# Optimization experiments

Measured on AMD Instinct MI355X. Metric: run time of the kernel, lower is better.

## Reference

```python
import jax, jax.numpy as jnp
import numpy as np

B, T = 65536, 200
H, S, P = 512, 1000, 5
EPS = 1e-6


def setup_inputs() -> dict:
    key = jax.random.key(0)
    ks = jax.random.split(key, 8)
    init = lambda k, shp, fan: (jax.random.normal(k, shp, jnp.float32) / np.float32(np.sqrt(fan)))
    return {
        "X": jax.random.randint(ks[0], (B,), 0, S, dtype=jnp.int32),
        "y": jax.random.randint(ks[1], (B, T), 0, 2, dtype=jnp.int32),
        "embed": init(ks[2], (S, H), 1.0),
        "W1": init(ks[3], (H, H), H), "b1": jnp.zeros((H,), jnp.float32),
        "W2": init(ks[4], (H, H), H), "b2": jnp.zeros((H,), jnp.float32),
        "Wout": init(ks[5], (H, P), H), "bout": jnp.zeros((P,), jnp.float32),
    }


def reference(X, y, embed, W1, b1, W2, b2, Wout, bout):
    # --- MLP over skill embeddings: params (B, 5) = (l, f, g, s, latent0) ---
    e = embed[X]                                    # (B, H)
    h = jax.nn.relu(e @ W1 + b1)                    # num_layers = 2
    h = jax.nn.relu(h @ W2 + b2)
    params = jnp.clip(jax.nn.sigmoid(h @ Wout + bout), EPS, 1.0 - EPS)  # (B, 5)
    l, g, s = params[:, 0], params[:, 2], params[:, 3]
    latent0 = params[:, 4]                          # (B,)

    y_clean = jnp.where(y == -1, 0, y).astype(jnp.float32)  # (B, T)

    # --- BKT latent-update recurrence over T steps ---
    def step(latent, y_t):
        num1 = latent * (1.0 - s)
        correct = num1 + (1.0 - latent) * g
        k_t1 = num1 / correct
        k_t0 = latent * s / (latent * s + (1.0 - latent) * (1.0 - g))
        k_t = jnp.where(y_t > 0.5, k_t1, k_t0)
        nxt = jnp.clip(k_t + (1.0 - k_t) * l, EPS, 1.0 - EPS)
        return nxt, (correct, latent)

    _, (corrects, latents) = jax.lax.scan(step, latent0, y_clean.T)  # (T, B) each
    return corrects.T, latents.T, params
```

## Files before the change

### kernel.cpp

```cpp
#include <hip/hip_runtime.h>


typedef unsigned int uint;
typedef unsigned char uchar;
typedef unsigned short ushort_t;
typedef __attribute__((ext_vector_type(8))) short short8;
typedef __attribute__((ext_vector_type(4))) float f32x4;
typedef __attribute__((ext_vector_type(2))) uint uint2v;

#define SS 1000
#define HH 512
#define TT 200
#define BB_ 65536
#define PP 5

#define OFF_EMB   0
#define OFF_B1    512000
#define OFF_B2    512512
#define OFF_WOUT  513024
#define OFF_BOUT  515584
#define CONV_TOT  515589

__device__ __forceinline__ float b2f(ushort_t u) {
    return __uint_as_float(((uint)u) << 16);
}
__device__ __forceinline__ ushort_t f2b(float f) {
    uint u = __float_as_uint(f);
    uint r = u + 0x7FFFu + ((u >> 16) & 1u);
    return (ushort_t)(r >> 16);
}
__device__ __forceinline__ int detect_bf16(const uint* __restrict__ embed_raw,
                                           int tid) {
    uint w = embed_raw[tid & 63];
    uint e = (w >> 7) & 0xFFu;
    bool pl = (e >= 117u && e <= 130u);
    return __popcll(__ballot(pl)) >= 32 ? 1 : 0;
}
__device__ __forceinline__ ushort_t ld_bf16(const void* src, int idx, int fb) {
    return fb ? ((const ushort_t*)src)[idx] : f2b(((const float*)src)[idx]);
}

__device__ __forceinline__ float bkt_step(float latent, bool yt,
                                          float oms, float omg, float A1,
                                          float A0, float g, float s,
                                          float oml, float l) {
    float num1    = latent * oms;
    float correct = fmaf(latent, A1, g);
    float lats    = latent * s;
    float num = yt ? num1 : lats;
    float den = yt ? correct : fmaf(latent, A0, omg);
    float kt  = num * __builtin_amdgcn_rcpf(den);
    float nxt = fmaf(kt, oml, l);
    return fminf(fmaxf(nxt, 1e-6f), 1.f - 1e-6f);
}

__global__ __launch_bounds__(256) void prep_kernel(
    const void* __restrict__ embed, const void* __restrict__ W1,
    const void* __restrict__ b1,    const void* __restrict__ W2,
    const void* __restrict__ b2,    const void* __restrict__ Wout,
    const void* __restrict__ bout,
    ushort_t* __restrict__ conv, ushort_t* __restrict__ WT1,
    ushort_t* __restrict__ WT2)
{
    int tid = threadIdx.x;
    int fb = detect_bf16((const uint*)embed, tid);
    int bx = blockIdx.x;
    if (bx < 504) {
        int i = (bx * 256 + tid) * 4;
        if (i < CONV_TOT) {
            const void* src; int off;
            if      (i < OFF_B1)   { src = embed; off = i; }
            else if (i < OFF_B2)   { src = b1;    off = i - OFF_B1; }
            else if (i < OFF_WOUT) { src = b2;    off = i - OFF_B2; }
            else if (i < OFF_BOUT) { src = Wout;  off = i - OFF_WOUT; }
            else                   { src = bout;  off = i - OFF_BOUT; }
            if (i + 3 < CONV_TOT) {
                ushort4 o;
                if (fb) {
                    o = *(const ushort4*)((const ushort_t*)src + off);
                } else {
                    float4 v = *(const float4*)((const float*)src + off);
                    o.x = f2b(v.x); o.y = f2b(v.y); o.z = f2b(v.z); o.w = f2b(v.w);
                }
                *(ushort4*)(conv + i) = o;
            } else {
                for (int k = 0; i + k < CONV_TOT; k++)
                    conv[i + k] = ld_bf16(src, off + k, fb);
            }
        }
    } else {
        __shared__ ushort_t t[32][33];
        int bi = bx - 504;
        const void* W = bi < 256 ? W1 : W2;
        ushort_t* WT = bi < 256 ? WT1 : WT2;
        int ti = bi & 255;
        int k0 = (ti & 15) * 32, n0 = (ti >> 4) * 32;
        int tx = tid & 31, ty = tid >> 5;
        #pragma unroll
        for (int i = ty; i < 32; i += 8)
            t[i][tx] = ld_bf16(W, (k0 + i) * HH + n0 + tx, fb);
        __syncthreads();
        #pragma unroll
        for (int i = ty; i < 32; i += 8)
            WT[(n0 + i) * HH + k0 + tx] = t[tx][i];
    }
}

__global__ __launch_bounds__(256) void mlp_layer(
    const ushort_t* __restrict__ A, const ushort_t* __restrict__ WT,
    const ushort_t* __restrict__ bias, ushort_t* __restrict__ H, int Mclamp)
{
    int tid = threadIdx.x;
    int lane = tid & 63;
    int wave = tid >> 6;
    int m_base = blockIdx.x * 64 + wave * 16;
    int n_base = blockIdx.y * 16;
    int lrow = lane & 15;
    int q = lane >> 4;
    int rowA = m_base + lrow; if (rowA > Mclamp) rowA = Mclamp;

    const short8* Ap = (const short8*)(A + (size_t)rowA * HH) + q;
    const short8* Bp = (const short8*)(WT + (size_t)(n_base + lrow) * HH) + q;

    f32x4 acc = {0.f, 0.f, 0.f, 0.f};
    #pragma unroll 8
    for (int kk = 0; kk < 16; kk++) {
        short8 a = Ap[kk * 4];
        short8 b = Bp[kk * 4];
        acc = __builtin_amdgcn_mfma_f32_16x16x32_bf16(a, b, acc, 0, 0, 0);
    }

    int orow = m_base + q * 4;
    int n = n_base + lrow;
    float bb = b2f(bias[n]);
    #pragma unroll
    for (int r = 0; r < 4; r++) {
        float v = acc[r] + bb;
        H[(size_t)(orow + r) * HH + n] = f2b(fmaxf(v, 0.f));
    }
}

__global__ __launch_bounds__(256) void params_kernel(
    const ushort_t* __restrict__ h2, const ushort_t* __restrict__ conv,
    float* __restrict__ table)
{
    int wid = blockIdx.x * 4 + (threadIdx.x >> 6);
    int lane = threadIdx.x & 63;
    if (wid >= SS * PP) return;
    int row = wid / PP, p = wid - row * PP;
    const ushort_t* Wout = conv + OFF_WOUT;
    const ushort_t* bout = conv + OFF_BOUT;
    const short8* hr = (const short8*)(h2 + (size_t)row * HH);
    short8 h = hr[lane];
    float acc = 0.f;
    #pragma unroll
    for (int j = 0; j < 8; j++) {
        int k = lane * 8 + j;
        acc += b2f((ushort_t)h[j]) * b2f(Wout[k * PP + p]);
    }
    #pragma unroll
    for (int m = 32; m; m >>= 1) acc += __shfl_xor(acc, m);
    if (lane == 0) {
        float x = acc + b2f(bout[p]);
        float sg = 1.f / (1.f + expf(-x));
        sg = fminf(fmaxf(sg, 1e-6f), 1.f - 1e-6f);
        table[(size_t)row * 8 + p] = sg;
    }
}

__global__ __launch_bounds__(256) void scan_a(
    const int* __restrict__ X, const int* __restrict__ y,
    const float* __restrict__ table,
    float* __restrict__ cpA, uint* __restrict__ maskA)
{
    __shared__ uchar ybit[128 * 50];
    int tid = threadIdx.x;
    int rbase = blockIdx.x * 128;

    for (int idx = tid; idx < 6400; idx += 256) {
        int r = idx / 50, k = idx - r * 50;
        int4 v = *(const int4*)(y + (size_t)(rbase + r) * TT + k * 4);
        ybit[r * 50 + k] = (uchar)((uint)(v.x == 1) | ((uint)(v.y == 1) << 1) |
                                   ((uint)(v.z == 1) << 2) | ((uint)(v.w == 1) << 3));
    }
    __syncthreads();

    if (tid < 128) {
        int rg = rbase + tid;
        int xi = X[rg]; xi = xi < 0 ? 0 : (xi >= SS ? SS - 1 : xi);
        float l      = table[xi * 8 + 0];
        float g      = table[xi * 8 + 2];
        float s      = table[xi * 8 + 3];
        float latent = table[xi * 8 + 4];
        float oms = 1.f - s, omg = 1.f - g, oml = 1.f - l;
        float A1 = 1.f - s - g, A0 = s + g - 1.f;
        const uchar* yb = &ybit[tid * 50];
        float cp[8]; uint mk[8];
        #pragma unroll
        for (int w = 0; w < 8; w++) {
            cp[w] = latent;
            uint m = 0;
            #pragma unroll
            for (int k = 0; k < 7; k++) {
                if (k * 4 >= 25) break;
                uint nib = yb[w * 25 / 4 + 0];
            }
            #pragma unroll
            for (int i = 0; i < 25; i++) {
                int t_ = w * 25 + i;
                uint bit = (ybit[tid * 50 + (t_ >> 2)] >> (t_ & 3)) & 1u;
                m |= bit << i;
                latent = bkt_step(latent, bit, oms, omg, A1, A0, g, s, oml, l);
            }
            mk[w] = m;
        }
        #pragma unroll
        for (int w = 0; w < 8; w++) {
            cpA[(size_t)w * BB_ + rg]   = cp[w];
            maskA[(size_t)w * BB_ + rg] = mk[w];
        }
    }
}

__global__ __launch_bounds__(256) void scan_b(
    const int* __restrict__ X, const float* __restrict__ table,
    const float* __restrict__ cpA, const uint* __restrict__ maskA,
    const uint* __restrict__ embed_raw, void* __restrict__ out)
{
    __shared__ __align__(16) float stg[32 * 200];
    __shared__ float pA1[32], pG[32];
    int tid = threadIdx.x;
    int rbase = blockIdx.x * 32;
    int fb = detect_bf16(embed_raw, tid);

    int r = tid >> 3, j = tid & 7;
    int rg = rbase + r;
    int xi = X[rg]; xi = xi < 0 ? 0 : (xi >= SS ? SS - 1 : xi);
    float l  = table[xi * 8 + 0];
    float p1 = table[xi * 8 + 1];
    float g  = table[xi * 8 + 2];
    float s  = table[xi * 8 + 3];
    float L0 = table[xi * 8 + 4];

    if (j == 0) { pA1[r] = 1.f - s - g; pG[r] = g; }

    if (j < 5) {
        float pv = j == 0 ? l : j == 1 ? p1 : j == 2 ? g : j == 3 ? s : L0;
        size_t po = 2ull * BB_ * TT + (size_t)rg * 5 + j;
        if (fb) ((ushort_t*)out)[po] = f2b(pv);
        else    ((float*)out)[po] = pv;
    }

    float latent = cpA[(size_t)j * BB_ + rg];
    uint  u      = maskA[(size_t)j * BB_ + rg];
    float oms = 1.f - s, omg = 1.f - g, oml = 1.f - l;
    float A1 = 1.f - s - g, A0 = s + g - 1.f;

    int sbase = r * 200 + j * 25;
    #pragma unroll
    for (int i = 0; i < 25; i++) {
        stg[sbase + i] = latent;
        latent = bkt_step(latent, (u >> i) & 1u,
                          oms, omg, A1, A0, g, s, oml, l);
    }
    __syncthreads();

    const f32x4* src = (const f32x4*)stg;
    if (!fb) {
        f32x4* dc = (f32x4*)((float*)out + (size_t)rbase * TT);
        f32x4* dl = (f32x4*)((float*)out + (size_t)BB_ * TT + (size_t)rbase * TT);
        for (int idx = tid; idx < 1600; idx += 256) {
            int rr = idx / 50;
            f32x4 v = src[idx];
            float a1 = pA1[rr], gg = pG[rr];
            f32x4 c;
            c[0] = fmaf(v[0], a1, gg); c[1] = fmaf(v[1], a1, gg);
            c[2] = fmaf(v[2], a1, gg); c[3] = fmaf(v[3], a1, gg);
            dl[idx] = v;
            dc[idx] = c;
        }
    } else {
        uint2v* dc = (uint2v*)((ushort_t*)out + (size_t)rbase * TT);
        uint2v* dl = (uint2v*)((ushort_t*)out + (size_t)BB_ * TT + (size_t)rbase * TT);
        for (int idx = tid; idx < 1600; idx += 256) {
            int rr = idx / 50;
            f32x4 v = src[idx];
            float a1 = pA1[rr], gg = pG[rr];
            uint2v lv, cv;
            lv[0] = (uint)f2b(v[0]) | ((uint)f2b(v[1]) << 16);
            lv[1] = (uint)f2b(v[2]) | ((uint)f2b(v[3]) << 16);
            cv[0] = (uint)f2b(fmaf(v[0], a1, gg)) | ((uint)f2b(fmaf(v[1], a1, gg)) << 16);
            cv[1] = (uint)f2b(fmaf(v[2], a1, gg)) | ((uint)f2b(fmaf(v[3], a1, gg)) << 16);
            dl[idx] = lv;
            dc[idx] = cv;
        }
    }
}

extern "C" void kernel_launch(void* const* d_in, const int* in_sizes, int n_in,
                              void* d_out, int out_size, void* d_ws, size_t ws_size,
                              hipStream_t stream) {
    const int* X = (const int*)d_in[0];
    const int* y = (const int*)d_in[1];

    char* ws = (char*)d_ws;
    ushort_t* conv  = (ushort_t*)(ws);
    ushort_t* WT1   = (ushort_t*)(ws + 1048576);
    ushort_t* WT2   = (ushort_t*)(ws + 1572864);
    ushort_t* h1    = (ushort_t*)(ws + 2097152);
    ushort_t* h2    = (ushort_t*)(ws + 3145728);
    float*    table = (float*)(ws + 4194304);
    float*    cpA   = (float*)(ws + 4227072);
    uint*     maskA = (uint*)(ws + 6324224);

    prep_kernel<<<dim3(1016, 1, 1), 256, 0, stream>>>(
        d_in[2], d_in[3], d_in[4], d_in[5], d_in[6], d_in[7], d_in[8],
        conv, WT1, WT2);
    mlp_layer<<<dim3(16, 32, 1), 256, 0, stream>>>(
        conv + OFF_EMB, WT1, conv + OFF_B1, h1, SS - 1);
    mlp_layer<<<dim3(16, 32, 1), 256, 0, stream>>>(
        h1, WT2, conv + OFF_B2, h2, 1023);
    params_kernel<<<dim3(1250, 1, 1), 256, 0, stream>>>(h2, conv, table);
    scan_a<<<dim3(512, 1, 1), 256, 0, stream>>>(X, y, table, cpA, maskA);
    scan_b<<<dim3(2048, 1, 1), 256, 0, stream>>>(
        X, table, cpA, maskA, (const uint*)d_in[2], (void*)d_out);
}
```

Measured before the change: 203.6 us.

## Fuse both MLP layers and output projection into one kernel with LDS-resident activations

Replaces two mlp_layer launches and params_kernel with a single mlp_fused kernel. Each block takes 16 rows, keeps the hidden activations in swizzled shared memory and computes layer 1, layer 2 and the 5-way output projection before writing the sigmoid table. This removes two kernel launches and the global round trips for h1 and h2. In exchange it runs only 63 blocks, each streaming the full W1 and W2 weights, so parallelism drops sharply and weight reads are repeated per block.

```diff
diff --git a/kernel.cpp b/kernel.cpp
--- a/kernel.cpp
+++ b/kernel.cpp
@@ -106,65 +106,99 @@
     }
 }
 
-__global__ __launch_bounds__(256) void mlp_layer(
-    const ushort_t* __restrict__ A, const ushort_t* __restrict__ WT,
-    const ushort_t* __restrict__ bias, ushort_t* __restrict__ H, int Mclamp)
+__global__ __launch_bounds__(256) void mlp_fused(
+    const ushort_t* __restrict__ conv, const ushort_t* __restrict__ WT1,
+    const ushort_t* __restrict__ WT2, float* __restrict__ table)
 {
-    int tid = threadIdx.x;
+    __shared__ __align__(16) ushort_t hbuf[16 * 512];
+    int tid  = threadIdx.x;
     int lane = tid & 63;
     int wave = tid >> 6;
-    int m_base = blockIdx.x * 64 + wave * 16;
-    int n_base = blockIdx.y * 16;
     int lrow = lane & 15;
-    int q = lane >> 4;
-    int rowA = m_base + lrow; if (rowA > Mclamp) rowA = Mclamp;
-
-    const short8* Ap = (const short8*)(A + (size_t)rowA * HH) + q;
-    const short8* Bp = (const short8*)(WT + (size_t)(n_base + lrow) * HH) + q;
-
-    f32x4 acc = {0.f, 0.f, 0.f, 0.f};
-    #pragma unroll 8
+    int q    = lane >> 4;
+
+    int R0 = blockIdx.x * 16;
+    int rowA = R0 + lrow; if (rowA > SS - 1) rowA = SS - 1;
+    int nw = wave * 128;
+
+    short8 af[16];
+    {
+        const short8* Ap = (const short8*)(conv + OFF_EMB + (size_t)rowA * HH) + q;
+        #pragma unroll
+        for (int kk = 0; kk < 16; kk++) af[kk] = Ap[kk * 4];
+    }
+    f32x4 acc[8];
+    #pragma unroll
+    for (int nt = 0; nt < 8; nt++) acc[nt] = (f32x4){0.f, 0.f, 0.f, 0.f};
+    #pragma unroll
+    for (int nt = 0; nt < 8; nt++) {
+        const short8* Bp = (const short8*)(WT1 + (size_t)(nw + nt * 16 + lrow) * HH) + q;
+        #pragma unroll
+        for (int kk = 0; kk < 16; kk++)
+            acc[nt] = __builtin_amdgcn_mfma_f32_16x16x32_bf16(af[kk], Bp[kk * 4],
+                                                              acc[nt], 0, 0, 0);
+    }
+    #pragma unroll
+    for (int nt = 0; nt < 8; nt++) {
+        int n = nw + nt * 16 + lrow;
+        float bb = b2f(conv[OFF_B1 + n]);
+        #pragma unroll
+        for (int r = 0; r < 4; r++) {
+            int rw = q * 4 + r;
+            hbuf[rw * 512 + (n ^ ((rw & 7) << 3))] = f2b(fmaxf(acc[nt][r] + bb, 0.f));
+        }
+    }
+    __syncthreads();
+
+    #pragma unroll
     for (int kk = 0; kk < 16; kk++) {
-        short8 a = Ap[kk * 4];
-        short8 b = Bp[kk * 4];
-        acc = __builtin_amdgcn_mfma_f32_16x16x32_bf16(a, b, acc, 0, 0, 0);
-    }
-
-    int orow = m_base + q * 4;
-    int n = n_base + lrow;
-    float bb = b2f(bias[n]);
-    #pragma unroll
-    for (int r = 0; r < 4; r++) {
-        float v = acc[r] + bb;
-        H[(size_t)(orow + r) * HH + n] = f2b(fmaxf(v, 0.f));
-    }
-}
-
-__global__ __launch_bounds__(256) void params_kernel(
-    const ushort_t* __restrict__ h2, const ushort_t* __restrict__ conv,
-    float* __restrict__ table)
-{
-    int wid = blockIdx.x * 4 + (threadIdx.x >> 6);
-    int lane = threadIdx.x & 63;
-    if (wid >= SS * PP) return;
-    int row = wid / PP, p = wid - row * PP;
+        int e0 = (kk * 32 + q * 8) ^ ((lrow & 7) << 3);
+        af[kk] = *(const short8*)&hbuf[lrow * 512 + e0];
+    }
+    __syncthreads();
+    #pragma unroll
+    for (int nt = 0; nt < 8; nt++) acc[nt] = (f32x4){0.f, 0.f, 0.f, 0.f};
+    #pragma unroll
+    for (int nt = 0; nt < 8; nt++) {
+        const short8* Bp = (const short8*)(WT2 + (size_t)(nw + nt * 16 + lrow) * HH) + q;
+        #pragma unroll
+        for (int kk = 0; kk < 16; kk++)
+            acc[nt] = __builtin_amdgcn_mfma_f32_16x16x32_bf16(af[kk], Bp[kk * 4],
+                                                              acc[nt], 0, 0, 0);
+    }
+    #pragma unroll
+    for (int nt = 0; nt < 8; nt++) {
+        int n = nw + nt * 16 + lrow;
+        float bb = b2f(conv[OFF_B2 + n]);
+        #pragma unroll
+        for (int r = 0; r < 4; r++) {
+            int rw = q * 4 + r;
+            hbuf[rw * 512 + (n ^ ((rw & 7) << 3))] = f2b(fmaxf(acc[nt][r] + bb, 0.f));
+        }
+    }
+    __syncthreads();
+
     const ushort_t* Wout = conv + OFF_WOUT;
     const ushort_t* bout = conv + OFF_BOUT;
-    const short8* hr = (const short8*)(h2 + (size_t)row * HH);
-    short8 h = hr[lane];
-    float acc = 0.f;
-    #pragma unroll
-    for (int j = 0; j < 8; j++) {
-        int k = lane * 8 + j;
-        acc += b2f((ushort_t)h[j]) * b2f(Wout[k * PP + p]);
-    }
-    #pragma unroll
-    for (int m = 32; m; m >>= 1) acc += __shfl_xor(acc, m);
-    if (lane == 0) {
-        float x = acc + b2f(bout[p]);
-        float sg = 1.f / (1.f + expf(-x));
-        sg = fminf(fmaxf(sg, 1e-6f), 1.f - 1e-6f);
-        table[(size_t)row * 8 + p] = sg;
+    #pragma unroll 1
+    for (int i = 0; i < 20; i++) {
+        int wid = wave + i * 4;
+        int row = wid / 5, p = wid - row * 5;
+        short8 h = *(const short8*)&hbuf[row * 512 + ((lane * 8) ^ ((row & 7) << 3))];
+        float acc1 = 0.f;
+        #pragma unroll
+        for (int j = 0; j < 8; j++) {
+            int k = lane * 8 + j;
+            acc1 += b2f((ushort_t)h[j]) * b2f(Wout[k * PP + p]);
+        }
+        #pragma unroll
+        for (int m = 32; m; m >>= 1) acc1 += __shfl_xor(acc1, m);
+        if (lane == 0 && R0 + row < SS) {
+            float x = acc1 + b2f(bout[p]);
+            float sg = 1.f / (1.f + expf(-x));
+            sg = fminf(fmaxf(sg, 1e-6f), 1.f - 1e-6f);
+            table[(size_t)(R0 + row) * 8 + p] = sg;
+        }
     }
 }
 
@@ -307,8 +341,6 @@
     ushort_t* conv  = (ushort_t*)(ws);
     ushort_t* WT1   = (ushort_t*)(ws + 1048576);
     ushort_t* WT2   = (ushort_t*)(ws + 1572864);
-    ushort_t* h1    = (ushort_t*)(ws + 2097152);
-    ushort_t* h2    = (ushort_t*)(ws + 3145728);
     float*    table = (float*)(ws + 4194304);
     float*    cpA   = (float*)(ws + 4227072);
     uint*     maskA = (uint*)(ws + 6324224);
@@ -316,11 +348,7 @@
     prep_kernel<<<dim3(1016, 1, 1), 256, 0, stream>>>(
         d_in[2], d_in[3], d_in[4], d_in[5], d_in[6], d_in[7], d_in[8],
         conv, WT1, WT2);
-    mlp_layer<<<dim3(16, 32, 1), 256, 0, stream>>>(
-        conv + OFF_EMB, WT1, conv + OFF_B1, h1, SS - 1);
-    mlp_layer<<<dim3(16, 32, 1), 256, 0, stream>>>(
-        h1, WT2, conv + OFF_B2, h2, 1023);
-    params_kernel<<<dim3(1250, 1, 1), 256, 0, stream>>>(h2, conv, table);
+    mlp_fused<<<dim3(63, 1, 1), 256, 0, stream>>>(conv, WT1, WT2, table);
     scan_a<<<dim3(512, 1, 1), 256, 0, stream>>>(X, y, table, cpA, maskA);
     scan_b<<<dim3(2048, 1, 1), 256, 0, stream>>>(
         X, table, cpA, maskA, (const uint*)d_in[2], (void*)d_out);
```

Result: slower. 231.2 us (+13.6%).

## Fuse two-pass BKT scan into a single kernel with one thread per row

Applied to the files above, without the earlier changes.

Replaces the two-pass scan, where a first kernel saved checkpoints and bitmasks and a second replayed eight segments in parallel, with one kernel. In it, 32 threads per block each run the full 200-step recurrence for one row, then all 128 threads write the staged results. This removes the intermediate checkpoint traffic and one launch. The cost is a serial 200-step dependency chain per thread, with only 32 active lanes per block during the scan, so latency may be exposed.

```diff
diff --git a/kernel.cpp b/kernel.cpp
--- a/kernel.cpp
+++ b/kernel.cpp
@@ -168,16 +168,19 @@
     }
 }
 
-__global__ __launch_bounds__(256) void scan_a(
+__global__ __launch_bounds__(128) void scan_one(
     const int* __restrict__ X, const int* __restrict__ y,
-    const float* __restrict__ table,
-    float* __restrict__ cpA, uint* __restrict__ maskA)
-{
-    __shared__ uchar ybit[128 * 50];
+    const float* __restrict__ table, const uint* __restrict__ embed_raw,
+    void* __restrict__ out)
+{
+    __shared__ __align__(16) float stg[32 * 200];
+    __shared__ uchar ybit[32 * 50];
+    __shared__ float pA1[32], pG[32];
     int tid = threadIdx.x;
-    int rbase = blockIdx.x * 128;
-
-    for (int idx = tid; idx < 6400; idx += 256) {
+    int rbase = blockIdx.x * 32;
+    int fb = detect_bf16(embed_raw, tid);
+
+    for (int idx = tid; idx < 1600; idx += 128) {
         int r = idx / 50, k = idx - r * 50;
         int4 v = *(const int4*)(y + (size_t)(rbase + r) * TT + k * 4);
         ybit[r * 50 + k] = (uchar)((uint)(v.x == 1) | ((uint)(v.y == 1) << 1) |
@@ -185,83 +188,37 @@
     }
     __syncthreads();
 
-    if (tid < 128) {
+    if (tid < 32) {
         int rg = rbase + tid;
         int xi = X[rg]; xi = xi < 0 ? 0 : (xi >= SS ? SS - 1 : xi);
         float l      = table[xi * 8 + 0];
+        float p1     = table[xi * 8 + 1];
         float g      = table[xi * 8 + 2];
         float s      = table[xi * 8 + 3];
         float latent = table[xi * 8 + 4];
+        pA1[tid] = 1.f - s - g;
+        pG[tid]  = g;
+
+        size_t po = 2ull * BB_ * TT + (size_t)rg * 5;
+        if (fb) {
+            ushort_t* op = (ushort_t*)out + po;
+            op[0] = f2b(l); op[1] = f2b(p1); op[2] = f2b(g);
+            op[3] = f2b(s); op[4] = f2b(latent);
+        } else {
+            float* op = (float*)out + po;
+            op[0] = l; op[1] = p1; op[2] = g; op[3] = s; op[4] = latent;
+        }
+
         float oms = 1.f - s, omg = 1.f - g, oml = 1.f - l;
         float A1 = 1.f - s - g, A0 = s + g - 1.f;
         const uchar* yb = &ybit[tid * 50];
-        float cp[8]; uint mk[8];
-        #pragma unroll
-        for (int w = 0; w < 8; w++) {
-            cp[w] = latent;
-            uint m = 0;
-            #pragma unroll
-            for (int k = 0; k < 7; k++) {
-                if (k * 4 >= 25) break;
-                uint nib = yb[w * 25 / 4 + 0];
-            }
-            #pragma unroll
-            for (int i = 0; i < 25; i++) {
-                int t_ = w * 25 + i;
-                uint bit = (ybit[tid * 50 + (t_ >> 2)] >> (t_ & 3)) & 1u;
-                m |= bit << i;
-                latent = bkt_step(latent, bit, oms, omg, A1, A0, g, s, oml, l);
-            }
-            mk[w] = m;
-        }
-        #pragma unroll
-        for (int w = 0; w < 8; w++) {
-            cpA[(size_t)w * BB_ + rg]   = cp[w];
-            maskA[(size_t)w * BB_ + rg] = mk[w];
-        }
-    }
-}
-
-__global__ __launch_bounds__(256) void scan_b(
-    const int* __restrict__ X, const float* __restrict__ table,
-    const float* __restrict__ cpA, const uint* __restrict__ maskA,
-    const uint* __restrict__ embed_raw, void* __restrict__ out)
-{
-    __shared__ __align__(16) float stg[32 * 200];
-    __shared__ float pA1[32], pG[32];
-    int tid = threadIdx.x;
-    int rbase = blockIdx.x * 32;
-    int fb = detect_bf16(embed_raw, tid);
-
-    int r = tid >> 3, j = tid & 7;
-    int rg = rbase + r;
-    int xi = X[rg]; xi = xi < 0 ? 0 : (xi >= SS ? SS - 1 : xi);
-    float l  = table[xi * 8 + 0];
-    float p1 = table[xi * 8 + 1];
-    float g  = table[xi * 8 + 2];
-    float s  = table[xi * 8 + 3];
-    float L0 = table[xi * 8 + 4];
-
-    if (j == 0) { pA1[r] = 1.f - s - g; pG[r] = g; }
-
-    if (j < 5) {
-        float pv = j == 0 ? l : j == 1 ? p1 : j == 2 ? g : j == 3 ? s : L0;
-        size_t po = 2ull * BB_ * TT + (size_t)rg * 5 + j;
-        if (fb) ((ushort_t*)out)[po] = f2b(pv);
-        else    ((float*)out)[po] = pv;
-    }
-
-    float latent = cpA[(size_t)j * BB_ + rg];
-    uint  u      = maskA[(size_t)j * BB_ + rg];
-    float oms = 1.f - s, omg = 1.f - g, oml = 1.f - l;
-    float A1 = 1.f - s - g, A0 = s + g - 1.f;
-
-    int sbase = r * 200 + j * 25;
-    #pragma unroll
-    for (int i = 0; i < 25; i++) {
-        stg[sbase + i] = latent;
-        latent = bkt_step(latent, (u >> i) & 1u,
-                          oms, omg, A1, A0, g, s, oml, l);
+        float* sp = &stg[tid * 200];
+        #pragma unroll 4
+        for (int t = 0; t < 200; t++) {
+            sp[t] = latent;
+            uint bit = (yb[t >> 2] >> (t & 3)) & 1u;
+            latent = bkt_step(latent, bit, oms, omg, A1, A0, g, s, oml, l);
+        }
     }
     __syncthreads();
 
@@ -269,7 +226,7 @@
     if (!fb) {
         f32x4* dc = (f32x4*)((float*)out + (size_t)rbase * TT);
         f32x4* dl = (f32x4*)((float*)out + (size_t)BB_ * TT + (size_t)rbase * TT);
-        for (int idx = tid; idx < 1600; idx += 256) {
+        for (int idx = tid; idx < 1600; idx += 128) {
             int rr = idx / 50;
             f32x4 v = src[idx];
             float a1 = pA1[rr], gg = pG[rr];
@@ -282,7 +239,7 @@
     } else {
         uint2v* dc = (uint2v*)((ushort_t*)out + (size_t)rbase * TT);
         uint2v* dl = (uint2v*)((ushort_t*)out + (size_t)BB_ * TT + (size_t)rbase * TT);
-        for (int idx = tid; idx < 1600; idx += 256) {
+        for (int idx = tid; idx < 1600; idx += 128) {
             int rr = idx / 50;
             f32x4 v = src[idx];
             float a1 = pA1[rr], gg = pG[rr];
@@ -310,8 +267,6 @@
     ushort_t* h1    = (ushort_t*)(ws + 2097152);
     ushort_t* h2    = (ushort_t*)(ws + 3145728);
     float*    table = (float*)(ws + 4194304);
-    float*    cpA   = (float*)(ws + 4227072);
-    uint*     maskA = (uint*)(ws + 6324224);
 
     prep_kernel<<<dim3(1016, 1, 1), 256, 0, stream>>>(
         d_in[2], d_in[3], d_in[4], d_in[5], d_in[6], d_in[7], d_in[8],
@@ -321,7 +276,6 @@
     mlp_layer<<<dim3(16, 32, 1), 256, 0, stream>>>(
         h1, WT2, conv + OFF_B2, h2, 1023);
     params_kernel<<<dim3(1250, 1, 1), 256, 0, stream>>>(h2, conv, table);
-    scan_a<<<dim3(512, 1, 1), 256, 0, stream>>>(X, y, table, cpA, maskA);
-    scan_b<<<dim3(2048, 1, 1), 256, 0, stream>>>(
-        X, table, cpA, maskA, (const uint*)d_in[2], (void*)d_out);
-}
+    scan_one<<<dim3(2048, 1, 1), 128, 0, stream>>>(
+        X, y, table, (const uint*)d_in[2], (void*)d_out);
+}
```

Measured after the change: 209.7 us. 3.0% more time.
